# Kernel tuning notes

Measured on AMD Instinct MI355X. Metric: run time of the kernel, lower is better.

## Reference

```python
import jax, jax.numpy as jnp
import numpy as np

NUM_USERS = 60000
NUM_ITEMS = 40000
N_NODES = NUM_USERS + NUM_ITEMS
EMBED_K = 128
E_HALF = 1_000_000  # bipartite interactions; symmetrized -> 2M directed edges


def setup_inputs() -> dict:
    key = jax.random.key(0)
    k1, k2, k3, k4, k5, k6, k7 = jax.random.split(key, 7)
    scale = 1.0 / np.sqrt(EMBED_K)  # ~ xavier_normal
    Gu = jax.random.normal(k1, (NUM_USERS, EMBED_K), jnp.float32) * scale
    Gi = jax.random.normal(k2, (NUM_ITEMS, EMBED_K), jnp.float32) * scale
    W0 = jax.random.normal(k3, (EMBED_K, EMBED_K), jnp.float32) * scale
    W1 = jax.random.normal(k4, (EMBED_K, EMBED_K), jnp.float32) * scale
    W2 = jax.random.normal(k5, (EMBED_K, EMBED_K), jnp.float32) * scale
    # bipartite user-item graph, symmetrized (items offset by NUM_USERS)
    u = jax.random.randint(k6, (E_HALF,), 0, NUM_USERS)
    it = jax.random.randint(k7, (E_HALF,), 0, NUM_ITEMS) + NUM_USERS
    src = jnp.concatenate([u, it])
    dst = jnp.concatenate([it, u])
    edge_index = jnp.stack([src, dst]).astype(jnp.int32)  # [2, 2M]
    return {"Gu": Gu, "Gi": Gi, "W0": W0, "W1": W1, "W2": W2,
            "edge_index": edge_index}


def reference(Gu, Gi, W0, W1, W2, edge_index):
    # add_self_loops=False, bias=False) -> ReLU), then split into (gu, gi).
    src, dst = edge_index[0], edge_index[1]
    n_users = Gu.shape[0]
    n_nodes = Gu.shape[0] + Gi.shape[0]
    # PyG gcn_norm (no self loops): deg = scatter(1, col); norm = d^-1/2[row]*d^-1/2[col]
    ones = jnp.ones(src.shape, Gu.dtype)
    deg = jax.ops.segment_sum(ones, dst, num_segments=n_nodes)
    dinv = jnp.where(deg > 0, jax.lax.rsqrt(jnp.maximum(deg, 1.0)), 0.0)
    norm = dinv[src] * dinv[dst]  # [E]
    x = jnp.concatenate([Gu, Gi], axis=0)  # [N, d]
    for W in (W0, W1, W2):
        h = x @ W                                   # [N, d] dense GEMM
        msg = h[src] * norm[:, None]                # [E, d] gather + scale
        x = jax.nn.relu(jax.ops.segment_sum(msg, dst, num_segments=n_nodes))
    return x[:n_users], x[n_users:]
```

## Files before the change

### kernel.cpp

```cpp
#include <hip/hip_runtime.h>
#include <hip/hip_bf16.h>

#define EMB 128
#define NPB 256
#define NB_PAD 512
#define CHUNK 4096
#define FILL_CAP 7168

typedef unsigned int uint32;
typedef unsigned long long uint64;
typedef __attribute__((ext_vector_type(8))) short bf16x8;
typedef __attribute__((ext_vector_type(4))) float f32x4;
typedef __attribute__((ext_vector_type(2))) float f32x2;

__device__ __forceinline__ ushort f2bf(float f) {
    uint32 u = __float_as_uint(f);
    return (ushort)((u + 0x7fff + ((u >> 16) & 1)) >> 16);
}
__device__ __forceinline__ uint32 pack_hi2(uint32 u0, uint32 u1) {
    return (u1 & 0xffff0000u) | (u0 >> 16);
}
__device__ __forceinline__ float blo(uint32 u) { return __uint_as_float(u << 16); }
__device__ __forceinline__ float bhi(uint32 u) { return __uint_as_float(u & 0xffff0000u); }


__global__ __launch_bounds__(256) void bucket_count_kernel(
    const int* __restrict__ dst, int* __restrict__ bucket_cnt, int E, int NB) {
    __shared__ int cnt[NB_PAD];
    int t = threadIdx.x;
    long e0 = (long)blockIdx.x * CHUNK;
    int n = E - (int)e0; if (n > CHUNK) n = CHUNK;
    for (int b = t; b < NB_PAD; b += 256) cnt[b] = 0;
    __syncthreads();
    #pragma unroll
    for (int i = 0; i < CHUNK / 256; i++) {
        int idx = t + i * 256;
        if (idx < n) atomicAdd(&cnt[dst[e0 + idx] >> 8], 1);
    }
    __syncthreads();
    for (int b = t; b < NB; b += 256)
        if (cnt[b] > 0) atomicAdd(&bucket_cnt[b], cnt[b]);
}

__global__ void bucket_scan_kernel(const int* __restrict__ bucket_cnt,
                                   int* __restrict__ ebase, int* __restrict__ gcursor,
                                   int NB, int E) {
    __shared__ int sc[512];
    int t = threadIdx.x;
    int v = (t < NB) ? bucket_cnt[t] : 0;
    sc[t] = v;
    __syncthreads();
    for (int off = 1; off < 512; off <<= 1) {
        int u = (t >= off) ? sc[t - off] : 0;
        __syncthreads();
        sc[t] += u;
        __syncthreads();
    }
    if (t < NB) {
        int excl = sc[t] - v;
        ebase[t] = excl;
        gcursor[t] = excl;
    }
    if (t == 0) ebase[NB] = E;
}


__global__ __launch_bounds__(256) void bucket_scatter_kernel(
    const int* __restrict__ src, const int* __restrict__ dst,
    int* __restrict__ gcursor, uint2* __restrict__ ebuf, int E, int NB) {
    __shared__ int cnt[NB_PAD];
    __shared__ int loff[NB_PAD];
    __shared__ int gbase[NB_PAD];
    __shared__ int pos[NB_PAD];
    __shared__ int sc[256];
    __shared__ uint2 stage[CHUNK];
    int t = threadIdx.x;
    long e0 = (long)blockIdx.x * CHUNK;
    int n = E - (int)e0; if (n > CHUNK) n = CHUNK;
    for (int b = t; b < NB_PAD; b += 256) { cnt[b] = 0; pos[b] = 0; }
    __syncthreads();
    int es[CHUNK / 256], ed[CHUNK / 256];
    #pragma unroll
    for (int i = 0; i < CHUNK / 256; i++) {
        int idx = t + i * 256;
        if (idx < n) {
            es[i] = src[e0 + idx];
            ed[i] = dst[e0 + idx];
            atomicAdd(&cnt[ed[i] >> 8], 1);
        }
    }
    __syncthreads();
    int a = cnt[2 * t], b2 = cnt[2 * t + 1];
    sc[t] = a + b2;
    __syncthreads();
    for (int off = 1; off < 256; off <<= 1) {
        int v = (t >= off) ? sc[t - off] : 0;
        __syncthreads();
        sc[t] += v;
        __syncthreads();
    }
    int excl = sc[t] - (a + b2);
    loff[2 * t] = excl;
    loff[2 * t + 1] = excl + a;
    __syncthreads();
    for (int b = t; b < NB; b += 256)
        if (cnt[b] > 0) gbase[b] = atomicAdd(&gcursor[b], cnt[b]);
    __syncthreads();
    #pragma unroll
    for (int i = 0; i < CHUNK / 256; i++) {
        int idx = t + i * 256;
        if (idx < n) {
            int b = ed[i] >> 8;
            int p = atomicAdd(&pos[b], 1);
            stage[loff[b] + p] = make_uint2((uint32)es[i], (uint32)ed[i]);
        }
    }
    __syncthreads();
    for (int b = t; b < NB; b += 256) {
        int c = cnt[b], lo = loff[b], go = gbase[b];
        for (int k = 0; k < c; k++) ebuf[go + k] = stage[lo + k];
    }
}


__global__ __launch_bounds__(256) void bucket_deg_kernel(
    const uint2* __restrict__ ebuf, const int* __restrict__ ebase,
    int* __restrict__ deg, float* __restrict__ dinv, int N) {
    __shared__ int cnt[NPB];
    int t = threadIdx.x;
    int n0 = blockIdx.x * NPB;
    int nn = N - n0; if (nn > NPB) nn = NPB;
    cnt[t] = 0;
    __syncthreads();
    int e0 = ebase[blockIdx.x];
    int e1 = ebase[blockIdx.x + 1];
    for (int e = e0 + t; e < e1; e += 256) {
        uint2 sd = ebuf[e];
        atomicAdd(&cnt[(int)sd.y - n0], 1);
    }
    __syncthreads();
    if (t < nn) {
        int c = cnt[t];
        deg[n0 + t] = c;
        dinv[n0 + t] = c > 0 ? rsqrtf((float)c) : 0.0f;
    }
}


__global__ void scan1_kernel(const int* __restrict__ deg, int* __restrict__ rowptr,
                             int* __restrict__ bsum, int N) {
    __shared__ int sc[256];
    int t = threadIdx.x;
    int base = blockIdx.x * 1024 + t * 4;
    int d0 = 0, d1 = 0, d2 = 0, d3 = 0;
    if (base + 3 < N) {
        int4 v = *(const int4*)(deg + base);
        d0 = v.x; d1 = v.y; d2 = v.z; d3 = v.w;
    } else {
        if (base     < N) d0 = deg[base];
        if (base + 1 < N) d1 = deg[base + 1];
        if (base + 2 < N) d2 = deg[base + 2];
        if (base + 3 < N) d3 = deg[base + 3];
    }
    int s = d0 + d1 + d2 + d3;
    sc[t] = s;
    __syncthreads();
    for (int off = 1; off < 256; off <<= 1) {
        int v = (t >= off) ? sc[t - off] : 0;
        __syncthreads();
        sc[t] += v;
        __syncthreads();
    }
    int excl = sc[t] - s;
    if (t == 255) bsum[blockIdx.x] = sc[255];
    int dd[4] = {d0, d1, d2, d3};
    int p = excl;
    #pragma unroll
    for (int j = 0; j < 4; j++) {
        int i = base + j;
        if (i < N) rowptr[i] = p;
        p += dd[j];
    }
}

__global__ void scan2_kernel(int* bsum, int nb) {
    __shared__ int sc[128];
    int t = threadIdx.x;
    int v = (t < nb) ? bsum[t] : 0;
    sc[t] = v;
    __syncthreads();
    for (int off = 1; off < 128; off <<= 1) {
        int u = (t >= off) ? sc[t - off] : 0;
        __syncthreads();
        sc[t] += u;
        __syncthreads();
    }
    if (t < nb) bsum[t] = sc[t] - v;
}

__global__ void scan3_kernel(int* __restrict__ rowptr, const int* __restrict__ bsum,
                             int N, int E) {
    int t = threadIdx.x, b = blockIdx.x;
    int add = bsum[b];
    int base = b * 1024 + t * 4;
    #pragma unroll
    for (int j = 0; j < 4; j++) {
        int i = base + j;
        if (i < N) rowptr[i] += add;
    }
    if (b == 0 && t == 0) rowptr[N] = E;
}


__global__ __launch_bounds__(256) void fill_ew_kernel(
    uint2* __restrict__ ebuf, const int* __restrict__ rowptr,
    const float* __restrict__ dinv, int N) {
    __shared__ uint2 stage[FILL_CAP];
    __shared__ int cnt[NPB];
    __shared__ int rp[NPB];
    int t = threadIdx.x;
    int n0 = blockIdx.x * NPB;
    int nn = N - n0; if (nn > NPB) nn = NPB;
    if (t < nn) { cnt[t] = 0; rp[t] = rowptr[n0 + t]; }
    __syncthreads();
    int e0 = rowptr[n0];
    int e1 = rowptr[n0 + nn];
    int ecount = e1 - e0; if (ecount > FILL_CAP) ecount = FILL_CAP;
    for (int o = t; o < ecount; o += 256) stage[o] = ebuf[e0 + o];
    __syncthreads();
    for (int o = t; o < ecount; o += 256) {
        uint2 sd = stage[o];
        int local = (int)sd.y - n0;
        int p = atomicAdd(&cnt[local], 1);
        int s = (int)sd.x;
        ebuf[rp[local] + p] = make_uint2((uint32)s, __float_as_uint(dinv[s]));
    }
}


#define GATH(k) p[k] = Yh[(size_t)rows[k] * 64 + lane]
#define FMA2(k) do { a0 += w[k] * blo(p[k]); a1 += w[k] * bhi(p[k]); } while (0)

__global__ __launch_bounds__(256) void agg_relu_kernel(
    const uint32* __restrict__ Yh,
    const int* __restrict__ rowptr, const uint2* __restrict__ ew,
    const float* __restrict__ dinv, float* __restrict__ out, int N) {
    int node = blockIdx.x * 4 + (threadIdx.x >> 6);
    if (node >= N) return;
    int lane = threadIdx.x & 63;
    int e0 = __builtin_amdgcn_readfirstlane(rowptr[node]);
    int e1 = __builtin_amdgcn_readfirstlane(rowptr[node + 1]);
    float a0 = 0.f, a1 = 0.f;
    int base = e0;
    for (; base + 16 <= e1; base += 16) {
        uint32 rows[16]; float w[16]; uint32 p[16];
        #pragma unroll
        for (int k = 0; k < 16; k++) {
            uint2 sw = ew[base + k];
            rows[k] = sw.x;
            w[k] = __uint_as_float(sw.y);
        }
        #pragma unroll
        for (int k = 0; k < 16; k++) GATH(k);
        #pragma unroll
        for (int k = 0; k < 16; k++) FMA2(k);
    }
    for (; base < e1; base += 8) {
        uint32 rows[8]; float w[8]; uint32 p[8];
        #pragma unroll
        for (int k = 0; k < 8; k++) {
            int e = (base + k < e1) ? base + k : e0;
            uint2 sw = ew[e];
            rows[k] = sw.x;
            w[k] = (base + k < e1) ? __uint_as_float(sw.y) : 0.0f;
        }
        #pragma unroll
        for (int k = 0; k < 8; k++) GATH(k);
        #pragma unroll
        for (int k = 0; k < 8; k++) FMA2(k);
    }
    float wd = dinv[node];
    f32x2 r;
    r.x = fmaxf(a0 * wd, 0.f);
    r.y = fmaxf(a1 * wd, 0.f);
    __builtin_nontemporal_store(r, (f32x2*)(out + (size_t)node * EMB + lane * 2));
}


__global__ void wsplit_kernel(const float* __restrict__ W0, const float* __restrict__ W1,
                              const float* __restrict__ W2,
                              ushort* __restrict__ Whi, ushort* __restrict__ Wlo) {
    const float* W = (blockIdx.x == 0) ? W0 : (blockIdx.x == 1) ? W1 : W2;
    ushort* hiT = Whi + blockIdx.x * EMB * EMB;
    ushort* loT = Wlo + blockIdx.x * EMB * EMB;
    for (int i = threadIdx.x; i < EMB * EMB; i += blockDim.x) {
        int k = i >> 7, n = i & 127;
        float w = W[i];
        uint32 u = __float_as_uint(w);
        ushort hi = (ushort)(u >> 16);
        float hif = __uint_as_float(u & 0xffff0000u);
        ushort lo = f2bf(w - hif);
        hiT[n * EMB + k] = hi;
        loT[n * EMB + k] = lo;
    }
}


union FragU { uint32 u[4]; bf16x8 v; };

__global__ __launch_bounds__(256, 2) void gemm_mfma_kernel(
    const float* __restrict__ A, const float* __restrict__ A2, int Msplit,
    const ushort* __restrict__ WhiT, const ushort* __restrict__ WloT,
    ushort* __restrict__ Yh, int M) {
    __shared__ float As[16][132];
    int t = threadIdx.x;
    int wv = t >> 6, lane = t & 63, quad = lane >> 4, l16 = lane & 15;

    FragU bfr[8][2];
    #pragma unroll
    for (int kc = 0; kc < 8; kc++) {
        const ushort* srcW = (kc < 4) ? WhiT : WloT;
        int kb = (kc & 3) * 32 + quad * 8;
        #pragma unroll
        for (int c = 0; c < 2; c++) {
            int n = wv * 32 + c * 16 + l16;
            const uint32* p = (const uint32*)(srcW + n * EMB + kb);
            bfr[kc][c].u[0] = p[0];
            bfr[kc][c].u[1] = p[1];
            bfr[kc][c].u[2] = p[2];
            bfr[kc][c].u[3] = p[3];
        }
    }

    int srow = t >> 4, skq = t & 15;
    int ntile = (M + 15) >> 4;
    for (int tile = blockIdx.x; tile < ntile; tile += (int)gridDim.x) {
        int r0 = tile << 4;
        __syncthreads();
        {
            float4 v0 = {0.f, 0.f, 0.f, 0.f}, v1 = v0;
            int row = r0 + srow;
            if (row < M) {
                const float* ga = (row < Msplit)
                    ? A  + (size_t)row * EMB + skq * 8
                    : A2 + (size_t)(row - Msplit) * EMB + skq * 8;
                v0 = *(const float4*)ga;
                v1 = *(const float4*)(ga + 4);
            }
            *(float4*)&As[srow][skq * 8] = v0;
            *(float4*)&As[srow][skq * 8 + 4] = v1;
        }
        __syncthreads();

        FragU ah[4], al[4];
        #pragma unroll
        for (int kc = 0; kc < 4; kc++) {
            const float* p = &As[l16][kc * 32 + quad * 8];
            float4 xa = *(const float4*)p;
            float4 xb = *(const float4*)(p + 4);
            uint32 u0 = __float_as_uint(xa.x), u1 = __float_as_uint(xa.y);
            uint32 u2 = __float_as_uint(xa.z), u3 = __float_as_uint(xa.w);
            uint32 u4 = __float_as_uint(xb.x), u5 = __float_as_uint(xb.y);
            uint32 u6 = __float_as_uint(xb.z), u7 = __float_as_uint(xb.w);
            ah[kc].u[0] = pack_hi2(u0, u1);
            ah[kc].u[1] = pack_hi2(u2, u3);
            ah[kc].u[2] = pack_hi2(u4, u5);
            ah[kc].u[3] = pack_hi2(u6, u7);
            float l0 = xa.x - __uint_as_float(u0 & 0xffff0000u);
            float l1 = xa.y - __uint_as_float(u1 & 0xffff0000u);
            float l2 = xa.z - __uint_as_float(u2 & 0xffff0000u);
            float l3 = xa.w - __uint_as_float(u3 & 0xffff0000u);
            float l4 = xb.x - __uint_as_float(u4 & 0xffff0000u);
            float l5 = xb.y - __uint_as_float(u5 & 0xffff0000u);
            float l6 = xb.z - __uint_as_float(u6 & 0xffff0000u);
            float l7 = xb.w - __uint_as_float(u7 & 0xffff0000u);
            al[kc].u[0] = pack_hi2(__float_as_uint(l0), __float_as_uint(l1));
            al[kc].u[1] = pack_hi2(__float_as_uint(l2), __float_as_uint(l3));
            al[kc].u[2] = pack_hi2(__float_as_uint(l4), __float_as_uint(l5));
            al[kc].u[3] = pack_hi2(__float_as_uint(l6), __float_as_uint(l7));
        }

        f32x4 acc0 = {0.f, 0.f, 0.f, 0.f};
        f32x4 acc1 = {0.f, 0.f, 0.f, 0.f};
        #pragma unroll
        for (int kc = 0; kc < 4; kc++) {
            acc0 = __builtin_amdgcn_mfma_f32_16x16x32_bf16(ah[kc].v, bfr[kc][0].v, acc0, 0, 0, 0);
            acc1 = __builtin_amdgcn_mfma_f32_16x16x32_bf16(ah[kc].v, bfr[kc][1].v, acc1, 0, 0, 0);
        }
        #pragma unroll
        for (int kc = 0; kc < 4; kc++) {
            acc0 = __builtin_amdgcn_mfma_f32_16x16x32_bf16(ah[kc].v, bfr[kc + 4][0].v, acc0, 0, 0, 0);
            acc1 = __builtin_amdgcn_mfma_f32_16x16x32_bf16(ah[kc].v, bfr[kc + 4][1].v, acc1, 0, 0, 0);
        }
        #pragma unroll
        for (int kc = 0; kc < 4; kc++) {
            acc0 = __builtin_amdgcn_mfma_f32_16x16x32_bf16(al[kc].v, bfr[kc][0].v, acc0, 0, 0, 0);
            acc1 = __builtin_amdgcn_mfma_f32_16x16x32_bf16(al[kc].v, bfr[kc][1].v, acc1, 0, 0, 0);
        }

        int colb = wv * 32 + l16;
        #pragma unroll
        for (int r = 0; r < 4; r++) {
            int row = r0 + quad * 4 + r;
            if (row < M) {
                Yh[(size_t)row * EMB + colb]      = f2bf(acc0[r]);
                Yh[(size_t)row * EMB + colb + 16] = f2bf(acc1[r]);
            }
        }
    }
}


extern "C" void kernel_launch(void* const* d_in, const int* in_sizes, int n_in,
                              void* d_out, int out_size, void* d_ws, size_t ws_size,
                              hipStream_t stream) {
    (void)n_in; (void)out_size; (void)ws_size;
    const float* Gu = (const float*)d_in[0];
    const float* Gi = (const float*)d_in[1];
    const float* W0 = (const float*)d_in[2];
    const float* W1 = (const float*)d_in[3];
    const float* W2 = (const float*)d_in[4];
    const int* ei = (const int*)d_in[5];

    int nu = in_sizes[0] / EMB;
    int ni = in_sizes[1] / EMB;
    int N = nu + ni;
    int E = in_sizes[5] / 2;
    const int* src = ei;
    const int* dst = ei + E;
    int NB = (N + NPB - 1) / NPB;

    ushort* Yh      = (ushort*)d_ws;
    uint2* ebuf     = (uint2*)(Yh + (size_t)N * EMB);
    int* deg        = (int*)(ebuf + (size_t)E);
    int* rowptr     = deg + N;
    float* dinv     = (float*)(rowptr + N + 1);
    int* bucket_cnt = (int*)(dinv + N);
    int* ebase      = bucket_cnt + NB;
    int* gcursor    = ebase + NB + 1;
    int* bsum       = gcursor + NB;
    ushort* WhiT    = (ushort*)(bsum + 128);
    ushort* WloT    = WhiT + 3 * EMB * EMB;
    float* X        = (float*)d_out;

    (void)hipMemsetAsync(bucket_cnt, 0, sizeof(int) * (size_t)NB, stream);

    wsplit_kernel<<<3, 256, 0, stream>>>(W0, W1, W2, WhiT, WloT);

    int ecb = (E + CHUNK - 1) / CHUNK;
    bucket_count_kernel<<<ecb, 256, 0, stream>>>(dst, bucket_cnt, E, NB);
    bucket_scan_kernel<<<1, 512, 0, stream>>>(bucket_cnt, ebase, gcursor, NB, E);
    bucket_scatter_kernel<<<ecb, 256, 0, stream>>>(src, dst, gcursor, ebuf, E, NB);
    bucket_deg_kernel<<<NB, 256, 0, stream>>>(ebuf, ebase, deg, dinv, N);
    int nb = (N + 1023) / 1024;
    scan1_kernel<<<nb, 256, 0, stream>>>(deg, rowptr, bsum, N);
    scan2_kernel<<<1, 128, 0, stream>>>(bsum, nb);
    scan3_kernel<<<nb, 256, 0, stream>>>(rowptr, bsum, N, E);
    fill_ew_kernel<<<NB, 256, 0, stream>>>(ebuf, rowptr, dinv, N);

    const uint2* ew = (const uint2*)ebuf;
    int aggBlocks = (N + 3) / 4;
    const int GB = 512;

    gemm_mfma_kernel<<<GB, 256, 0, stream>>>(Gu, Gi, nu, WhiT, WloT, Yh, N);
    agg_relu_kernel<<<aggBlocks, 256, 0, stream>>>((const uint32*)Yh, rowptr, ew, dinv, X, N);
    gemm_mfma_kernel<<<GB, 256, 0, stream>>>(X, X, N, WhiT + EMB * EMB, WloT + EMB * EMB, Yh, N);
    agg_relu_kernel<<<aggBlocks, 256, 0, stream>>>((const uint32*)Yh, rowptr, ew, dinv, X, N);
    gemm_mfma_kernel<<<GB, 256, 0, stream>>>(X, X, N, WhiT + 2 * EMB * EMB, WloT + 2 * EMB * EMB, Yh, N);
    agg_relu_kernel<<<aggBlocks, 256, 0, stream>>>((const uint32*)Yh, rowptr, ew, dinv, X, N);
}
```

Before: 468.8 us.

## Fuse aggregation+ReLU with next layer's MFMA GEMM into one kernel

Adds agg_gemm_kernel, in which each block aggregates and ReLUs 16 node rows into shared memory. It then multiplies that tile by the next layer's split-bf16 weights with MFMA and writes bf16 Yh directly. This removes the fp32 X write and re-read between layers, plus two kernel launches. Yh ping-pongs between the workspace and the unused second half of the output buffer. The costs are a block-wide sync between the gather and GEMM phases, and weight fragments reloaded per 16-row tile instead of held across many tiles.

```diff
diff --git a/kernel.cpp b/kernel.cpp
--- a/kernel.cpp
+++ b/kernel.cpp
@@ -241,6 +241,40 @@
 #define GATH(k) p[k] = Yh[(size_t)rows[k] * 64 + lane]
 #define FMA2(k) do { a0 += w[k] * blo(p[k]); a1 += w[k] * bhi(p[k]); } while (0)
 
+__device__ __forceinline__ void agg_node(
+    const uint32* __restrict__ Yh, const uint2* __restrict__ ew,
+    int e0, int e1, int lane, float& a0, float& a1) {
+    int base = e0;
+    for (; base + 16 <= e1; base += 16) {
+        uint32 rows[16]; float w[16]; uint32 p[16];
+        #pragma unroll
+        for (int k = 0; k < 16; k++) {
+            uint2 sw = ew[base + k];
+            rows[k] = sw.x;
+            w[k] = __uint_as_float(sw.y);
+        }
+        #pragma unroll
+        for (int k = 0; k < 16; k++) GATH(k);
+        #pragma unroll
+        for (int k = 0; k < 16; k++) FMA2(k);
+    }
+    for (; base < e1; base += 8) {
+        uint32 rows[8]; float w[8]; uint32 p[8];
+        #pragma unroll
+        for (int k = 0; k < 8; k++) {
+            int e = (base + k < e1) ? base + k : e0;
+            uint2 sw = ew[e];
+            rows[k] = sw.x;
+            w[k] = (base + k < e1) ? __uint_as_float(sw.y) : 0.0f;
+        }
+        #pragma unroll
+        for (int k = 0; k < 8; k++) GATH(k);
+        #pragma unroll
+        for (int k = 0; k < 8; k++) FMA2(k);
+    }
+}
+
+
 __global__ __launch_bounds__(256) void agg_relu_kernel(
     const uint32* __restrict__ Yh,
     const int* __restrict__ rowptr, const uint2* __restrict__ ew,
@@ -251,39 +285,106 @@
     int e0 = __builtin_amdgcn_readfirstlane(rowptr[node]);
     int e1 = __builtin_amdgcn_readfirstlane(rowptr[node + 1]);
     float a0 = 0.f, a1 = 0.f;
-    int base = e0;
-    for (; base + 16 <= e1; base += 16) {
-        uint32 rows[16]; float w[16]; uint32 p[16];
-        #pragma unroll
-        for (int k = 0; k < 16; k++) {
-            uint2 sw = ew[base + k];
-            rows[k] = sw.x;
-            w[k] = __uint_as_float(sw.y);
-        }
-        #pragma unroll
-        for (int k = 0; k < 16; k++) GATH(k);
-        #pragma unroll
-        for (int k = 0; k < 16; k++) FMA2(k);
-    }
-    for (; base < e1; base += 8) {
-        uint32 rows[8]; float w[8]; uint32 p[8];
-        #pragma unroll
-        for (int k = 0; k < 8; k++) {
-            int e = (base + k < e1) ? base + k : e0;
-            uint2 sw = ew[e];
-            rows[k] = sw.x;
-            w[k] = (base + k < e1) ? __uint_as_float(sw.y) : 0.0f;
-        }
-        #pragma unroll
-        for (int k = 0; k < 8; k++) GATH(k);
-        #pragma unroll
-        for (int k = 0; k < 8; k++) FMA2(k);
-    }
+    agg_node(Yh, ew, e0, e1, lane, a0, a1);
     float wd = dinv[node];
     f32x2 r;
     r.x = fmaxf(a0 * wd, 0.f);
     r.y = fmaxf(a1 * wd, 0.f);
     __builtin_nontemporal_store(r, (f32x2*)(out + (size_t)node * EMB + lane * 2));
+}
+
+
+union FragU { uint32 u[4]; bf16x8 v; };
+
+__global__ __launch_bounds__(256) void agg_gemm_kernel(
+    const uint32* __restrict__ Yin,
+    const int* __restrict__ rowptr, const uint2* __restrict__ ew,
+    const float* __restrict__ dinv,
+    const ushort* __restrict__ WhiT, const ushort* __restrict__ WloT,
+    ushort* __restrict__ Yout, int N) {
+    __shared__ float As[16][132];
+    int t = threadIdx.x;
+    int wv = t >> 6, lane = t & 63;
+    int r0 = blockIdx.x << 4;
+
+    #pragma unroll
+    for (int j = 0; j < 4; j++) {
+        int node = r0 + wv * 4 + j;
+        float a0 = 0.f, a1 = 0.f;
+        if (node < N) {
+            int e0 = __builtin_amdgcn_readfirstlane(rowptr[node]);
+            int e1 = __builtin_amdgcn_readfirstlane(rowptr[node + 1]);
+            agg_node(Yin, ew, e0, e1, lane, a0, a1);
+            float wd = dinv[node];
+            a0 = fmaxf(a0 * wd, 0.f);
+            a1 = fmaxf(a1 * wd, 0.f);
+        }
+        f32x2 r; r.x = a0; r.y = a1;
+        *(f32x2*)&As[wv * 4 + j][lane * 2] = r;
+    }
+    __syncthreads();
+
+    int quad = lane >> 4, l16 = lane & 15;
+    f32x4 acc0 = {0.f, 0.f, 0.f, 0.f};
+    f32x4 acc1 = {0.f, 0.f, 0.f, 0.f};
+    #pragma unroll
+    for (int kc = 0; kc < 4; kc++) {
+        int kb = kc * 32 + quad * 8;
+        FragU bh0, bh1, bl0, bl1;
+        {
+            const uint32* ph0 = (const uint32*)(WhiT + (wv * 32 + l16) * EMB + kb);
+            const uint32* ph1 = (const uint32*)(WhiT + (wv * 32 + 16 + l16) * EMB + kb);
+            const uint32* pl0 = (const uint32*)(WloT + (wv * 32 + l16) * EMB + kb);
+            const uint32* pl1 = (const uint32*)(WloT + (wv * 32 + 16 + l16) * EMB + kb);
+            #pragma unroll
+            for (int i = 0; i < 4; i++) {
+                bh0.u[i] = ph0[i]; bh1.u[i] = ph1[i];
+                bl0.u[i] = pl0[i]; bl1.u[i] = pl1[i];
+            }
+        }
+        FragU ah, al;
+        {
+            const float* p = &As[l16][kb];
+            float4 xa = *(const float4*)p;
+            float4 xb = *(const float4*)(p + 4);
+            uint32 u0 = __float_as_uint(xa.x), u1 = __float_as_uint(xa.y);
+            uint32 u2 = __float_as_uint(xa.z), u3 = __float_as_uint(xa.w);
+            uint32 u4 = __float_as_uint(xb.x), u5 = __float_as_uint(xb.y);
+            uint32 u6 = __float_as_uint(xb.z), u7 = __float_as_uint(xb.w);
+            ah.u[0] = pack_hi2(u0, u1);
+            ah.u[1] = pack_hi2(u2, u3);
+            ah.u[2] = pack_hi2(u4, u5);
+            ah.u[3] = pack_hi2(u6, u7);
+            float l0 = xa.x - __uint_as_float(u0 & 0xffff0000u);
+            float l1 = xa.y - __uint_as_float(u1 & 0xffff0000u);
+            float l2 = xa.z - __uint_as_float(u2 & 0xffff0000u);
+            float l3 = xa.w - __uint_as_float(u3 & 0xffff0000u);
+            float l4 = xb.x - __uint_as_float(u4 & 0xffff0000u);
+            float l5 = xb.y - __uint_as_float(u5 & 0xffff0000u);
+            float l6 = xb.z - __uint_as_float(u6 & 0xffff0000u);
+            float l7 = xb.w - __uint_as_float(u7 & 0xffff0000u);
+            al.u[0] = pack_hi2(__float_as_uint(l0), __float_as_uint(l1));
+            al.u[1] = pack_hi2(__float_as_uint(l2), __float_as_uint(l3));
+            al.u[2] = pack_hi2(__float_as_uint(l4), __float_as_uint(l5));
+            al.u[3] = pack_hi2(__float_as_uint(l6), __float_as_uint(l7));
+        }
+        acc0 = __builtin_amdgcn_mfma_f32_16x16x32_bf16(ah.v, bh0.v, acc0, 0, 0, 0);
+        acc1 = __builtin_amdgcn_mfma_f32_16x16x32_bf16(ah.v, bh1.v, acc1, 0, 0, 0);
+        acc0 = __builtin_amdgcn_mfma_f32_16x16x32_bf16(ah.v, bl0.v, acc0, 0, 0, 0);
+        acc1 = __builtin_amdgcn_mfma_f32_16x16x32_bf16(ah.v, bl1.v, acc1, 0, 0, 0);
+        acc0 = __builtin_amdgcn_mfma_f32_16x16x32_bf16(al.v, bh0.v, acc0, 0, 0, 0);
+        acc1 = __builtin_amdgcn_mfma_f32_16x16x32_bf16(al.v, bh1.v, acc1, 0, 0, 0);
+    }
+
+    int colb = wv * 32 + l16;
+    #pragma unroll
+    for (int r = 0; r < 4; r++) {
+        int row = r0 + quad * 4 + r;
+        if (row < N) {
+            Yout[(size_t)row * EMB + colb]      = f2bf(acc0[r]);
+            Yout[(size_t)row * EMB + colb + 16] = f2bf(acc1[r]);
+        }
+    }
 }
 
 
@@ -305,8 +406,6 @@
     }
 }
 
-
-union FragU { uint32 u[4]; bf16x8 v; };
 
 __global__ __launch_bounds__(256, 2) void gemm_mfma_kernel(
     const float* __restrict__ A, const float* __restrict__ A2, int Msplit,
@@ -430,8 +529,8 @@
     const int* dst = ei + E;
     int NB = (N + NPB - 1) / NPB;
 
-    ushort* Yh      = (ushort*)d_ws;
-    uint2* ebuf     = (uint2*)(Yh + (size_t)N * EMB);
+    ushort* Yh_a    = (ushort*)d_ws;
+    uint2* ebuf     = (uint2*)(Yh_a + (size_t)N * EMB);
     int* deg        = (int*)(ebuf + (size_t)E);
     int* rowptr     = deg + N;
     float* dinv     = (float*)(rowptr + N + 1);
@@ -441,6 +540,7 @@
     int* bsum       = gcursor + NB;
     ushort* WhiT    = (ushort*)(bsum + 128);
     ushort* WloT    = WhiT + 3 * EMB * EMB;
+    ushort* Yh_b    = (ushort*)d_out + (size_t)N * EMB;
     float* X        = (float*)d_out;
 
     (void)hipMemsetAsync(bucket_cnt, 0, sizeof(int) * (size_t)NB, stream);
@@ -460,12 +560,13 @@
 
     const uint2* ew = (const uint2*)ebuf;
     int aggBlocks = (N + 3) / 4;
+    int ntile = (N + 15) / 16;
     const int GB = 512;
 
-    gemm_mfma_kernel<<<GB, 256, 0, stream>>>(Gu, Gi, nu, WhiT, WloT, Yh, N);
-    agg_relu_kernel<<<aggBlocks, 256, 0, stream>>>((const uint32*)Yh, rowptr, ew, dinv, X, N);
-    gemm_mfma_kernel<<<GB, 256, 0, stream>>>(X, X, N, WhiT + EMB * EMB, WloT + EMB * EMB, Yh, N);
-    agg_relu_kernel<<<aggBlocks, 256, 0, stream>>>((const uint32*)Yh, rowptr, ew, dinv, X, N);
-    gemm_mfma_kernel<<<GB, 256, 0, stream>>>(X, X, N, WhiT + 2 * EMB * EMB, WloT + 2 * EMB * EMB, Yh, N);
-    agg_relu_kernel<<<aggBlocks, 256, 0, stream>>>((const uint32*)Yh, rowptr, ew, dinv, X, N);
-}
+    gemm_mfma_kernel<<<GB, 256, 0, stream>>>(Gu, Gi, nu, WhiT, WloT, Yh_a, N);
+    agg_gemm_kernel<<<ntile, 256, 0, stream>>>((const uint32*)Yh_a, rowptr, ew, dinv,
+                                               WhiT + EMB * EMB, WloT + EMB * EMB, Yh_b, N);
+    agg_gemm_kernel<<<ntile, 256, 0, stream>>>((const uint32*)Yh_b, rowptr, ew, dinv,
+                                               WhiT + 2 * EMB * EMB, WloT + 2 * EMB * EMB, Yh_a, N);
+    agg_relu_kernel<<<aggBlocks, 256, 0, stream>>>((const uint32*)Yh_a, rowptr, ew, dinv, X, N);
+}
```

New measurement: 499.8 us. 6.6% more time.
